# Optimization experiments

Measured on AMD Instinct MI355X. Metric: run time of the kernel, lower is better.

The kernel has to match this reference:

```python
import jax, jax.numpy as jnp
import numpy as np

L_LAYERS = 4
N_HEAD = 16
D_MODEL = 1024
D_K = 64
D_V = 64
D_HID = 4096
D_OUT = 10000
SEQ = 512
BATCH = 16
MASK_RATE = 0.15
LN_EPS = 1e-5


def sinusoid_table(n_position, model_size):
    pos = np.arange(n_position)[:, None]
    hid = np.arange(model_size)[None, :]
    angle = pos / np.power(10000, 2 * (hid // 2) / model_size)
    tab = np.array(angle)
    tab[:, 0::2] = np.sin(tab[:, 0::2])
    tab[:, 1::2] = np.cos(tab[:, 1::2])
    return jnp.asarray(tab, dtype=jnp.float32)


def layer_norm(x, w, b):
    mu = jnp.mean(x, axis=-1, keepdims=True)
    var = jnp.mean(jnp.square(x - mu), axis=-1, keepdims=True)
    return (x - mu) * jax.lax.rsqrt(var + LN_EPS) * w + b


def setup_inputs() -> dict:
    key = jax.random.key(0)
    ks = jax.random.split(key, 32)
    s = 0.02
    inp = {
        "x": jax.random.normal(ks[0], (SEQ, BATCH, D_MODEL), dtype=jnp.float32),
        "rnd": jax.random.uniform(ks[1], (BATCH, SEQ), dtype=jnp.float32),
        "posi": sinusoid_table(SEQ, D_MODEL),
        "ln0_w": jnp.ones((D_MODEL,), jnp.float32),
        "ln0_b": jnp.zeros((D_MODEL,), jnp.float32),
        # stacked per-layer params [L, ...]
        "Wq": jax.random.normal(ks[2], (L_LAYERS, N_HEAD * D_K, D_MODEL), jnp.float32) * np.sqrt(2.0 / (D_MODEL + D_K)),
        "bq": jnp.zeros((L_LAYERS, N_HEAD * D_K), jnp.float32),
        "Wk": jax.random.normal(ks[3], (L_LAYERS, N_HEAD * D_K, D_MODEL), jnp.float32) * np.sqrt(2.0 / (D_MODEL + D_K)),
        "bk": jnp.zeros((L_LAYERS, N_HEAD * D_K), jnp.float32),
        "Wv": jax.random.normal(ks[4], (L_LAYERS, N_HEAD * D_V, D_MODEL), jnp.float32) * np.sqrt(2.0 / (D_MODEL + D_V)),
        "bv": jnp.zeros((L_LAYERS, N_HEAD * D_V), jnp.float32),
        "Wfc": jax.random.normal(ks[5], (L_LAYERS, D_MODEL, N_HEAD * D_V), jnp.float32) * s,
        "bfc": jnp.zeros((L_LAYERS, D_MODEL), jnp.float32),
        "ln1_w": jnp.ones((L_LAYERS, D_MODEL), jnp.float32),
        "ln1_b": jnp.zeros((L_LAYERS, D_MODEL), jnp.float32),
        "W1": jax.random.normal(ks[6], (L_LAYERS, D_HID, D_MODEL), jnp.float32) * s,
        "b1": jnp.zeros((L_LAYERS, D_HID), jnp.float32),
        "W2": jax.random.normal(ks[7], (L_LAYERS, D_MODEL, D_HID), jnp.float32) * s,
        "b2": jnp.zeros((L_LAYERS, D_MODEL), jnp.float32),
        "ln2_w": jnp.ones((L_LAYERS, D_MODEL), jnp.float32),
        "ln2_b": jnp.zeros((L_LAYERS, D_MODEL), jnp.float32),
        "Wo": jax.random.normal(ks[8], (D_OUT, D_MODEL), jnp.float32) * s,
        "bo": jnp.zeros((D_OUT,), jnp.float32),
    }
    return inp


def reference(x, rnd, posi, ln0_w, ln0_b, Wq, bq, Wk, bk, Wv, bv, Wfc, bfc,
              ln1_w, ln1_b, W1, b1, W2, b2, ln2_w, ln2_b, Wo, bo):
    scale = 1.0 / np.sqrt(D_K)
    # [length, batch, d] -> [batch, length, d]
    h = jnp.transpose(x, (1, 0, 2))
    # random input masking: keep where rnd > mask_rate
    keep = (rnd > MASK_RATE).astype(h.dtype)  # [B, S]
    h = h * keep[:, :, None]
    enc = layer_norm(h, ln0_w, ln0_b) + posi[None, :, :]

    for l in range(L_LAYERS):
        residual = enc
        q = (enc @ Wq[l].T + bq[l]).reshape(BATCH, SEQ, N_HEAD, D_K)
        k = (enc @ Wk[l].T + bk[l]).reshape(BATCH, SEQ, N_HEAD, D_K)
        v = (enc @ Wv[l].T + bv[l]).reshape(BATCH, SEQ, N_HEAD, D_V)
        attn = jnp.einsum('bqhd,bkhd->bhqk', q, k) * scale
        attn = jax.nn.softmax(attn, axis=-1)
        out = jnp.einsum('bhqk,bkhd->bqhd', attn, v).reshape(BATCH, SEQ, N_HEAD * D_V)
        out = out @ Wfc[l].T + bfc[l]
        enc = layer_norm(out + residual, ln1_w[l], ln1_b[l])
        # position-wise FFN (conv1d kernel=1 == per-token linear)
        ff = jax.nn.relu(enc @ W1[l].T + b1[l]) @ W2[l].T + b2[l]
        enc = layer_norm(ff + enc, ln2_w[l], ln2_b[l])

    logits = enc @ Wo.T + bo  # [B, S, D_OUT]
    out = jax.nn.log_softmax(logits, axis=-1)
    return jnp.transpose(out, (1, 0, 2))  # [S, B, D_OUT]
```

## Files before the change

### kernel.cpp

```cpp
#include <hip/hip_runtime.h>
#include <cstdint>

typedef unsigned short u16;
typedef unsigned int u32;
typedef __attribute__((ext_vector_type(8))) short vs8;
typedef __attribute__((ext_vector_type(4))) short vs4;
typedef __attribute__((ext_vector_type(4))) float vf4;
typedef __attribute__((ext_vector_type(4))) float f32x4;

#define NLAYER 4
#define SEQ 512
#define BATCH 16
#define DM 1024
#define NTOK 8192
#define DOUT 10000
#define DOUTP 10240

static __device__ __forceinline__ u16 f2bf(float f) {
    u32 u = __float_as_uint(f);
    return (u16)((u + 0x7FFFu + ((u >> 16) & 1u)) >> 16);
}
static __device__ __forceinline__ float bf2f(u16 h) { return __uint_as_float((u32)h << 16); }

static __device__ __forceinline__ void gload16(const void* g, void* l) {
    __builtin_amdgcn_global_load_lds(
        (const __attribute__((address_space(1))) u32*)(uintptr_t)g,
        (__attribute__((address_space(3))) u32*)(u32)(uintptr_t)l, 16, 0, 0);
}

template <int BM, bool RELU, bool OUTBF>
__global__ __launch_bounds__(512, 1) void gemm2p(const u16* __restrict__ A, const u16* __restrict__ Bw,
                                                 const float* __restrict__ bias, void* __restrict__ Cv,
                                                 int N, int K, int nMt, int nNt)
{
    constexpr int LA = BM / 128;
    constexpr int LB = 2;
    constexpr int WCNT = 2 * (LA + LB);
    constexpr int MR = BM / 32;

    __shared__ __align__(16) u16 lds[2 * 2 * BM * 32 + 2 * 2 * 256 * 32];
    u16* As = lds;
    u16* Bs = lds + 2 * 2 * BM * 32;

    const int t = threadIdx.x;
    const int wid = t >> 6, lane = t & 63;
    const int lr = lane & 15, lg = lane >> 4;
    const int wr = wid >> 2, wc = wid & 3;
    const int wrb = wr * (BM / 2), wcb = wc * 64;
    const int slot8 = (lg ^ ((lr >> 1) & 3)) * 8;

    const int nwg = nMt * nNt;
    const int orig = blockIdx.x;
    const int q8 = nwg >> 3, r8 = nwg & 7;
    const int xcd = orig & 7, idx = orig >> 3;
    const int wg = ((xcd < r8) ? xcd * (q8 + 1) : r8 * (q8 + 1) + (xcd - r8) * q8) + idx;
    const int GN = 8;
    const int gsz = GN * nMt;
    const int grp = wg / gsz;
    const int rem = wg - grp * gsz;
    const int gw = min(GN, nNt - grp * GN);
    const int mt = rem / gw;
    const int nt = grp * GN + (rem - mt * gw);
    const size_t m0 = (size_t)mt * BM;
    const size_t n0 = (size_t)nt * 256;

    const int srow = wid * 16 + (lane >> 2);
    const int scg = (lane & 3) ^ ((lane >> 3) & 3);
    const u16* gA = A + (m0 + srow) * (size_t)K + scg * 8;
    const u16* gB = Bw + (n0 + srow) * (size_t)K + scg * 8;

    auto stageA = [&](int b, int kh, int kt) {
#pragma unroll
        for (int i = 0; i < LA; ++i)
            gload16(gA + (size_t)i * 128 * K + kt + kh * 32,
                    &As[(((b << 1) + kh) * BM + (i * 8 + wid) * 16) * 32]);
    };
    auto stageB = [&](int b, int kh, int kt) {
#pragma unroll
        for (int i = 0; i < LB; ++i)
            gload16(gB + (size_t)i * 128 * K + kt + kh * 32,
                    &Bs[(((b << 1) + kh) * 256 + (i * 8 + wid) * 16) * 32]);
    };
    auto ldA = [&](int i, int kk, int b) -> vs8 {
        return *(const vs8*)&As[(((b << 1) + kk) * BM + wrb + i * 16 + lr) * 32 + slot8];
    };
    auto ldB = [&](int j, int kk, int b) -> vs8 {
        return *(const vs8*)&Bs[(((b << 1) + kk) * 256 + wcb + j * 16 + lr) * 32 + slot8];
    };

    f32x4 acc[MR][4];
#pragma unroll
    for (int i = 0; i < MR; ++i)
#pragma unroll
        for (int j = 0; j < 4; ++j) acc[i][j] = (f32x4){0.f, 0.f, 0.f, 0.f};

    const int NT = K >> 6;

    stageA(0, 0, 0); stageB(0, 0, 0);
    stageA(0, 1, 0); stageB(0, 1, 0);
    stageA(1, 0, 64); stageB(1, 0, 64);
    if constexpr (WCNT == 8) asm volatile("s_waitcnt vmcnt(8)" ::: "memory");
    else                     asm volatile("s_waitcnt vmcnt(6)" ::: "memory");
    __builtin_amdgcn_s_barrier();

    for (int tt = 0; tt < NT; ++tt) {
        const int buf = tt & 1;
        const int ktn = min(tt + 1, NT - 1) << 6;
        const int ktn2 = min(tt + 2, NT - 1) << 6;
        vs8 af[MR], bf[4];

#pragma unroll
        for (int j = 0; j < 4; ++j) bf[j] = ldB(j, 0, buf);
#pragma unroll
        for (int i = 0; i < MR; ++i) af[i] = ldA(i, 0, buf);
        stageA(buf ^ 1, 1, ktn);
        stageB(buf ^ 1, 1, ktn);
        __builtin_amdgcn_s_barrier();
        asm volatile("s_waitcnt lgkmcnt(0)" ::: "memory");
        __builtin_amdgcn_sched_barrier(0);
        __builtin_amdgcn_s_setprio(1);
#pragma unroll
        for (int i = 0; i < MR; ++i)
#pragma unroll
            for (int j = 0; j < 4; ++j)
                acc[i][j] = __builtin_amdgcn_mfma_f32_16x16x32_bf16(bf[j], af[i], acc[i][j], 0, 0, 0);
        __builtin_amdgcn_s_setprio(0);
        if constexpr (WCNT == 8) asm volatile("s_waitcnt vmcnt(8)" ::: "memory");
        else                     asm volatile("s_waitcnt vmcnt(6)" ::: "memory");
        __builtin_amdgcn_s_barrier();

#pragma unroll
        for (int j = 0; j < 4; ++j) bf[j] = ldB(j, 1, buf);
#pragma unroll
        for (int i = 0; i < MR; ++i) af[i] = ldA(i, 1, buf);
        stageA(buf, 0, ktn2);
        stageB(buf, 0, ktn2);
        __builtin_amdgcn_s_barrier();
        asm volatile("s_waitcnt lgkmcnt(0)" ::: "memory");
        __builtin_amdgcn_sched_barrier(0);
        __builtin_amdgcn_s_setprio(1);
#pragma unroll
        for (int i = 0; i < MR; ++i)
#pragma unroll
            for (int j = 0; j < 4; ++j)
                acc[i][j] = __builtin_amdgcn_mfma_f32_16x16x32_bf16(bf[j], af[i], acc[i][j], 0, 0, 0);
        __builtin_amdgcn_s_setprio(0);
        if constexpr (WCNT == 8) asm volatile("s_waitcnt vmcnt(8)" ::: "memory");
        else                     asm volatile("s_waitcnt vmcnt(6)" ::: "memory");
        __builtin_amdgcn_s_barrier();
    }

    asm volatile("s_waitcnt vmcnt(0)" ::: "memory");

#pragma unroll
    for (int i = 0; i < MR; ++i) {
        const size_t cm = m0 + wrb + 16 * i + lr;
#pragma unroll
        for (int j = 0; j < 4; ++j) {
            const size_t cn = n0 + wcb + 16 * j + lg * 4;
            const vf4 bv4 = *(const vf4*)&bias[cn];
            f32x4 v = acc[i][j];
#pragma unroll
            for (int r = 0; r < 4; ++r) {
                v[r] += bv4[r];
                if (RELU) v[r] = fmaxf(v[r], 0.f);
            }
            if (OUTBF) {
                vs4 o;
#pragma unroll
                for (int r = 0; r < 4; ++r) o[r] = (short)f2bf(v[r]);
                *(vs4*)&((u16*)Cv)[cm * (size_t)N + cn] = o;
            } else {
                *(vf4*)&((float*)Cv)[cm * (size_t)N + cn] = v;
            }
        }
    }
}

__global__ __launch_bounds__(256) void vtrans_k(const u16* __restrict__ vb, u16* __restrict__ vt, int ldv)
{
    __shared__ u16 tile[64][80];
    const int t = threadIdx.x;
    const int bh = blockIdx.x >> 3, st = blockIdx.x & 7;
    const int b = bh >> 4, h = bh & 15;
    const int s0 = st * 64;
    {
        const int s = t >> 2, d0 = (t & 3) * 16;
        const vs8* src = (const vs8*)(vb + ((size_t)(b * 512 + s0 + s)) * ldv + h * 64 + d0);
        *(vs8*)&tile[s][d0] = src[0];
        *(vs8*)&tile[s][d0 + 8] = src[1];
    }
    __syncthreads();
    {
        const int d = t >> 2, r0 = (t & 3) * 16;
        u16 tmp[16];
#pragma unroll
        for (int i = 0; i < 16; ++i) tmp[i] = tile[r0 + i][d];
        vs8* dst = (vs8*)(vt + ((size_t)bh * 64 + d) * 512 + s0 + r0);
        dst[0] = *(const vs8*)&tmp[0];
        dst[1] = *(const vs8*)&tmp[8];
    }
}

__global__ __launch_bounds__(256) void attn_k(const u16* __restrict__ qb, const u16* __restrict__ kb,
                                              const u16* __restrict__ vtb, u16* __restrict__ ob, int ldq)
{
    __shared__ __align__(16) float SlF[32 * 520];
    const int t = threadIdx.x;
    const int wid = t >> 6, lane = t & 63;
    const int lr = lane & 15, lg = lane >> 4;
    const int bh = blockIdx.x >> 4, qt = blockIdx.x & 15;
    const int b = bh >> 4, h = bh & 15;
    const int q0 = qt * 32;

    vs8 aq[2][2];
#pragma unroll
    for (int i2 = 0; i2 < 2; ++i2)
#pragma unroll
        for (int kk = 0; kk < 2; ++kk)
            aq[i2][kk] = *(const vs8*)(qb + ((size_t)(b * 512 + q0 + 16 * i2 + lr)) * ldq + h * 64 + kk * 32 + lg * 8);

    f32x4 sa[2][8];
#pragma unroll
    for (int i2 = 0; i2 < 2; ++i2)
#pragma unroll
        for (int j = 0; j < 8; ++j) sa[i2][j] = (f32x4){0.f, 0.f, 0.f, 0.f};

#pragma unroll
    for (int j = 0; j < 8; ++j) {
        const int col = 128 * wid + 16 * j + lr;
#pragma unroll
        for (int kk = 0; kk < 2; ++kk) {
            vs8 bk = *(const vs8*)(kb + ((size_t)(b * 512 + col)) * ldq + h * 64 + kk * 32 + lg * 8);
#pragma unroll
            for (int i2 = 0; i2 < 2; ++i2)
                sa[i2][j] = __builtin_amdgcn_mfma_f32_16x16x32_bf16(bk, aq[i2][kk], sa[i2][j], 0, 0, 0);
        }
    }
#pragma unroll
    for (int i2 = 0; i2 < 2; ++i2)
#pragma unroll
        for (int j = 0; j < 8; ++j) {
            vf4 w;
#pragma unroll
            for (int r = 0; r < 4; ++r) w[r] = sa[i2][j][r] * 0.125f;
            *(vf4*)&SlF[(16 * i2 + lr) * 520 + 128 * wid + 16 * j + 4 * lg] = w;
        }
    __syncthreads();

    {
        const int row = t >> 3, seg = t & 7;
        const float* Sr = &SlF[row * 520 + seg * 64];
        float v[64];
        float m = -3.0e38f;
#pragma unroll
        for (int c = 0; c < 16; ++c) {
            const int cc = (c + row + seg) & 15;
            const vf4 w = *(const vf4*)&Sr[cc * 4];
#pragma unroll
            for (int e = 0; e < 4; ++e) { v[c * 4 + e] = w[e]; m = fmaxf(m, w[e]); }
        }
        m = fmaxf(m, __shfl_xor(m, 1));
        m = fmaxf(m, __shfl_xor(m, 2));
        m = fmaxf(m, __shfl_xor(m, 4));
        float s = 0.f;
#pragma unroll
        for (int i = 0; i < 64; ++i) { v[i] = __expf(v[i] - m); s += v[i]; }
        s += __shfl_xor(s, 1);
        s += __shfl_xor(s, 2);
        s += __shfl_xor(s, 4);
        const float inv = 1.f / s;
        u16* P16 = (u16*)SlF;
#pragma unroll
        for (int c = 0; c < 16; ++c) {
            const int cc = (c + row + seg) & 15;
            vs4 o;
#pragma unroll
            for (int e = 0; e < 4; ++e) o[e] = (short)f2bf(v[c * 4 + e] * inv);
            *(vs4*)&P16[row * 1040 + seg * 64 + cc * 4] = o;
        }
    }
    __syncthreads();

    const int rt = wid >> 1, ct0 = (wid & 1) * 2;
    f32x4 oa[2];
    oa[0] = (f32x4){0.f, 0.f, 0.f, 0.f};
    oa[1] = (f32x4){0.f, 0.f, 0.f, 0.f};
    const u16* P16 = (const u16*)SlF;
#pragma unroll
    for (int kt = 0; kt < 16; ++kt) {
        vs8 pa = *(const vs8*)&P16[(16 * rt + lr) * 1040 + kt * 32 + lg * 8];
#pragma unroll
        for (int c = 0; c < 2; ++c) {
            const int col = (ct0 + c) * 16 + lr;
            vs8 bv = *(const vs8*)(vtb + ((size_t)bh * 64 + col) * 512 + kt * 32 + lg * 8);
            oa[c] = __builtin_amdgcn_mfma_f32_16x16x32_bf16(bv, pa, oa[c], 0, 0, 0);
        }
    }
#pragma unroll
    for (int c = 0; c < 2; ++c) {
        const int qq = q0 + 16 * rt + lr;
        const int d0c = h * 64 + (ct0 + c) * 16 + lg * 4;
        vs4 o;
#pragma unroll
        for (int r = 0; r < 4; ++r) o[r] = (short)f2bf(oa[c][r]);
        *(vs4*)&ob[((size_t)b * 512 + qq) * 1024 + d0c] = o;
    }
}

__global__ __launch_bounds__(256) void embed_k(const float* __restrict__ x, const float* __restrict__ rnd,
                                               const float* __restrict__ posi, const float* __restrict__ w,
                                               const float* __restrict__ bb, u16* __restrict__ outb)
{
    const int tok = blockIdx.x;
    const int b = tok >> 9, s = tok & 511;
    const int t = threadIdx.x;
    const float keep = rnd[tok] > 0.15f ? 1.f : 0.f;
    vf4 xv = ((const vf4*)(x + ((size_t)s * 16 + b) * 1024))[t];
    xv *= keep;
    float s1 = xv[0] + xv[1] + xv[2] + xv[3];
    float s2 = xv[0] * xv[0] + xv[1] * xv[1] + xv[2] * xv[2] + xv[3] * xv[3];
#pragma unroll
    for (int mk = 1; mk < 64; mk <<= 1) { s1 += __shfl_xor(s1, mk); s2 += __shfl_xor(s2, mk); }
    __shared__ float red[8];
    if ((t & 63) == 0) { red[t >> 6] = s1; red[4 + (t >> 6)] = s2; }
    __syncthreads();
    s1 = red[0] + red[1] + red[2] + red[3];
    s2 = red[4] + red[5] + red[6] + red[7];
    const float mu = s1 * (1.f / 1024.f);
    const float var = s2 * (1.f / 1024.f) - mu * mu;
    const float rs = rsqrtf(var + 1e-5f);
    vf4 wv = ((const vf4*)w)[t];
    vf4 bv = ((const vf4*)bb)[t];
    vf4 pv = ((const vf4*)(posi + (size_t)s * 1024))[t];
    vs4 yb;
#pragma unroll
    for (int c = 0; c < 4; ++c)
        yb[c] = (short)f2bf((xv[c] - mu) * rs * wv[c] + bv[c] + pv[c]);
    *(vs4*)(outb + (size_t)tok * 1024 + t * 4) = yb;
}

__global__ __launch_bounds__(256) void add_ln_k(const u16* x, const u16* resid,
                                                const float* __restrict__ w, const float* __restrict__ bb,
                                                u16* out)
{
    const size_t row = blockIdx.x;
    const int t = threadIdx.x;
    const vs4 xv4 = *(const vs4*)(x + row * 1024 + t * 4);
    const vs4 rv4 = *(const vs4*)(resid + row * 1024 + t * 4);
    float xv[4];
#pragma unroll
    for (int c = 0; c < 4; ++c) xv[c] = bf2f((u16)xv4[c]) + bf2f((u16)rv4[c]);
    float s1 = xv[0] + xv[1] + xv[2] + xv[3];
    float s2 = xv[0] * xv[0] + xv[1] * xv[1] + xv[2] * xv[2] + xv[3] * xv[3];
#pragma unroll
    for (int mk = 1; mk < 64; mk <<= 1) { s1 += __shfl_xor(s1, mk); s2 += __shfl_xor(s2, mk); }
    __shared__ float red[8];
    if ((t & 63) == 0) { red[t >> 6] = s1; red[4 + (t >> 6)] = s2; }
    __syncthreads();
    s1 = red[0] + red[1] + red[2] + red[3];
    s2 = red[4] + red[5] + red[6] + red[7];
    const float mu = s1 * (1.f / 1024.f);
    const float var = s2 * (1.f / 1024.f) - mu * mu;
    const float rs = rsqrtf(var + 1e-5f);
    const vf4 wv = ((const vf4*)w)[t];
    const vf4 bv = ((const vf4*)bb)[t];
    vs4 yb;
#pragma unroll
    for (int c = 0; c < 4; ++c)
        yb[c] = (short)f2bf((xv[c] - mu) * rs * wv[c] + bv[c]);
    *(vs4*)(out + row * 1024 + t * 4) = yb;
}

__global__ __launch_bounds__(256) void logsm_k(const u16* __restrict__ lgts, float* __restrict__ out)
{
    const int tok = blockIdx.x;
    const int b = tok >> 9, s = tok & 511;
    const int t = threadIdx.x;
    const u16* row = lgts + (size_t)tok * DOUTP;
    float v[40];
    float m = -3.0e38f;
#pragma unroll
    for (int i = 0; i < 40; ++i) {
        const int c = t + 256 * i;
        v[i] = (c < DOUT) ? bf2f(row[c]) : -3.0e38f;
        m = fmaxf(m, v[i]);
    }
#pragma unroll
    for (int mk = 1; mk < 64; mk <<= 1) m = fmaxf(m, __shfl_xor(m, mk));
    __shared__ float red[8];
    if ((t & 63) == 0) red[t >> 6] = m;
    __syncthreads();
    m = fmaxf(fmaxf(red[0], red[1]), fmaxf(red[2], red[3]));
    float sum = 0.f;
#pragma unroll
    for (int i = 0; i < 40; ++i) sum += __expf(v[i] - m);
#pragma unroll
    for (int mk = 1; mk < 64; mk <<= 1) sum += __shfl_xor(sum, mk);
    if ((t & 63) == 0) red[4 + (t >> 6)] = sum;
    __syncthreads();
    sum = red[4] + red[5] + red[6] + red[7];
    const float ls = m + __logf(sum);
    float* orow = out + ((size_t)s * 16 + b) * DOUT;
#pragma unroll
    for (int i = 0; i < 40; ++i) {
        const int c = t + 256 * i;
        if (c < DOUT) __builtin_nontemporal_store(v[i] - ls, &orow[c]);
    }
}

__global__ void conv_k(const float* __restrict__ src, u16* __restrict__ dst, int n4)
{
    const int i = blockIdx.x * 256 + threadIdx.x;
    if (i >= n4) return;
    vf4 v = ((const vf4*)src)[i];
    vs4 o;
#pragma unroll
    for (int c = 0; c < 4; ++c) o[c] = (short)f2bf(v[c]);
    ((vs4*)dst)[i] = o;
}

__global__ void convq_k(const float* __restrict__ src, u16* __restrict__ dst, int n4, int perl4,
                        int dstl4, int off4)
{
    const int i = blockIdx.x * 256 + threadIdx.x;
    if (i >= n4) return;
    const int l = i / perl4, r = i - l * perl4;
    vf4 v = ((const vf4*)src)[i];
    vs4 o;
#pragma unroll
    for (int c = 0; c < 4; ++c) o[c] = (short)f2bf(v[c]);
    ((vs4*)dst)[(size_t)l * dstl4 + off4 + r] = o;
}

__global__ void biasq_k(const float* __restrict__ bq, const float* __restrict__ bk,
                        const float* __restrict__ bv, float* __restrict__ dst)
{
    const int i = blockIdx.x * 256 + threadIdx.x;
    const int l2 = i / 3072, c = i - l2 * 3072;
    float v;
    if (c < 1024) v = bq[l2 * 1024 + c];
    else if (c < 2048) v = bk[l2 * 1024 + c - 1024];
    else v = bv[l2 * 1024 + c - 2048];
    dst[i] = v;
}

__global__ void padwo_k(const float* __restrict__ src, u16* __restrict__ dst)
{
    const int i = blockIdx.x * 256 + threadIdx.x;
    const size_t e = (size_t)i * 4;
    const int r = (int)(e >> 10);
    vs4 o;
    if (r < DOUT) {
        vf4 v = *(const vf4*)(src + (size_t)r * 1024 + (e & 1023));
#pragma unroll
        for (int c = 0; c < 4; ++c) o[c] = (short)f2bf(v[c]);
    } else {
        o[0] = o[1] = o[2] = o[3] = 0;
    }
    *(vs4*)(dst + e) = o;
}

__global__ void padbo_k(const float* __restrict__ src, float* __restrict__ dst)
{
    const int i = blockIdx.x * 256 + threadIdx.x;
    if (i < DOUTP) dst[i] = (i < DOUT) ? src[i] : 0.f;
}

extern "C" void kernel_launch(void* const* d_in, const int* in_sizes, int n_in,
                              void* d_out, int out_size, void* d_ws, size_t ws_size,
                              hipStream_t stream)
{
    (void)in_sizes; (void)n_in; (void)out_size; (void)ws_size;
    const float* x     = (const float*)d_in[0];
    const float* rnd   = (const float*)d_in[1];
    const float* posi  = (const float*)d_in[2];
    const float* ln0_w = (const float*)d_in[3];
    const float* ln0_b = (const float*)d_in[4];
    const float* Wq    = (const float*)d_in[5];
    const float* bq    = (const float*)d_in[6];
    const float* Wk    = (const float*)d_in[7];
    const float* bk    = (const float*)d_in[8];
    const float* Wv    = (const float*)d_in[9];
    const float* bv    = (const float*)d_in[10];
    const float* Wfc   = (const float*)d_in[11];
    const float* bfc   = (const float*)d_in[12];
    const float* ln1_w = (const float*)d_in[13];
    const float* ln1_b = (const float*)d_in[14];
    const float* W1    = (const float*)d_in[15];
    const float* b1    = (const float*)d_in[16];
    const float* W2    = (const float*)d_in[17];
    const float* b2    = (const float*)d_in[18];
    const float* ln2_w = (const float*)d_in[19];
    const float* ln2_b = (const float*)d_in[20];
    const float* Wo    = (const float*)d_in[21];
    const float* bo    = (const float*)d_in[22];

    const size_t l1e = 1024 * 1024;
    const size_t l2e = 4096 * 1024;
    const size_t l3e = 3072 * 1024;

    char* p = (char*)d_ws;
    size_t off = 0;
    auto take = [&](size_t bytes) {
        char* r = p + off;
        off += (bytes + 255) & ~(size_t)255;
        return r;
    };
    u16*   Wqkv_b = (u16*)take(NLAYER * l3e * 2);
    u16*   Wfc_b  = (u16*)take(NLAYER * l1e * 2);
    u16*   W1_b   = (u16*)take(NLAYER * l2e * 2);
    u16*   W2_b   = (u16*)take(NLAYER * l2e * 2);
    u16*   Wo_b   = (u16*)take((size_t)DOUTP * DM * 2);
    float* bqkv_p = (float*)take(NLAYER * 3072 * 4);
    float* bo_p   = (float*)take(DOUTP * 4);
    u16*   enc_b  = (u16*)take((size_t)NTOK * DM * 2);
    char*  pool   = take((size_t)NTOK * DOUTP * 2);
    u16*   qkv_b  = (u16*)(pool);
    u16*   vt_b   = (u16*)(pool + 50331648);
    u16*   attn_b = (u16*)(pool + 67108864);
    u16*   fc_b   = (u16*)(pool);
    u16*   ff_b   = (u16*)(pool);
    u16*   ff2_b  = (u16*)(pool + 67108864);
    u16*   lgt_b  = (u16*)(pool);

    const dim3 blk(256);
    int n4;
    n4 = (int)(NLAYER * l1e / 4);
    convq_k<<<(n4 + 255) / 256, blk, 0, stream>>>(Wq, Wqkv_b, n4, 262144, 786432, 0);
    convq_k<<<(n4 + 255) / 256, blk, 0, stream>>>(Wk, Wqkv_b, n4, 262144, 786432, 262144);
    convq_k<<<(n4 + 255) / 256, blk, 0, stream>>>(Wv, Wqkv_b, n4, 262144, 786432, 524288);
    conv_k<<<(n4 + 255) / 256, blk, 0, stream>>>(Wfc, Wfc_b, n4);
    n4 = (int)(NLAYER * l2e / 4);
    conv_k<<<(n4 + 255) / 256, blk, 0, stream>>>(W1, W1_b, n4);
    conv_k<<<(n4 + 255) / 256, blk, 0, stream>>>(W2, W2_b, n4);
    padwo_k<<<(DOUTP * DM / 4) / 256, blk, 0, stream>>>(Wo, Wo_b);
    padbo_k<<<40, blk, 0, stream>>>(bo, bo_p);
    biasq_k<<<48, blk, 0, stream>>>(bq, bk, bv, bqkv_p);

    embed_k<<<NTOK, blk, 0, stream>>>(x, rnd, posi, ln0_w, ln0_b, enc_b);

    for (int l = 0; l < NLAYER; ++l) {
        gemm2p<128, false, true><<<768, 512, 0, stream>>>(enc_b, Wqkv_b + l * l3e, bqkv_p + l * 3072,
                                                          qkv_b, 3072, 1024, 64, 12);
        vtrans_k<<<2048, blk, 0, stream>>>(qkv_b + 2048, vt_b, 3072);
        attn_k<<<4096, blk, 0, stream>>>(qkv_b, qkv_b + 1024, vt_b, attn_b, 3072);
        gemm2p<128, false, true><<<256, 512, 0, stream>>>(attn_b, Wfc_b + l * l1e, bfc + l * 1024,
                                                          fc_b, 1024, 1024, 64, 4);
        add_ln_k<<<NTOK, blk, 0, stream>>>(fc_b, enc_b, ln1_w + l * 1024, ln1_b + l * 1024, enc_b);
        gemm2p<256, true, true><<<512, 512, 0, stream>>>(enc_b, W1_b + l * l2e, b1 + l * 4096,
                                                         ff_b, 4096, 1024, 32, 16);
        gemm2p<128, false, true><<<256, 512, 0, stream>>>(ff_b, W2_b + l * l2e, b2 + l * 1024,
                                                          ff2_b, 1024, 4096, 64, 4);
        add_ln_k<<<NTOK, blk, 0, stream>>>(ff2_b, enc_b, ln2_w + l * 1024, ln2_b + l * 1024, enc_b);
    }

    gemm2p<256, false, true><<<1280, 512, 0, stream>>>(enc_b, Wo_b, bo_p, lgt_b, DOUTP, 1024, 32, 40);
    logsm_k<<<NTOK, blk, 0, stream>>>(lgt_b, (float*)d_out);
}
```

Measured before the change: 2.086 ms.

## Fuse V transpose into GEMM epilogue, merge prep kernels, vectorize log-softmax

```diff
diff --git a/kernel.cpp b/kernel.cpp
--- a/kernel.cpp
+++ b/kernel.cpp
@@ -28,7 +28,7 @@
         (__attribute__((address_space(3))) u32*)(u32)(uintptr_t)l, 16, 0, 0);
 }
 
-template <int BM, bool RELU, bool OUTBF>
+template <int BM, bool RELU, bool OUTBF, bool TRV = false>
 __global__ __launch_bounds__(512, 1) void gemm2p(const u16* __restrict__ A, const u16* __restrict__ Bw,
                                                  const float* __restrict__ bias, void* __restrict__ Cv,
                                                  int N, int K, int nMt, int nNt)
@@ -122,8 +122,12 @@
 #pragma unroll
         for (int i = 0; i < MR; ++i)
 #pragma unroll
-            for (int j = 0; j < 4; ++j)
-                acc[i][j] = __builtin_amdgcn_mfma_f32_16x16x32_bf16(bf[j], af[i], acc[i][j], 0, 0, 0);
+            for (int j = 0; j < 4; ++j) {
+                if constexpr (TRV)
+                    acc[i][j] = __builtin_amdgcn_mfma_f32_16x16x32_bf16(af[i], bf[j], acc[i][j], 0, 0, 0);
+                else
+                    acc[i][j] = __builtin_amdgcn_mfma_f32_16x16x32_bf16(bf[j], af[i], acc[i][j], 0, 0, 0);
+            }
         __builtin_amdgcn_s_setprio(0);
         if constexpr (WCNT == 8) asm volatile("s_waitcnt vmcnt(8)" ::: "memory");
         else                     asm volatile("s_waitcnt vmcnt(6)" ::: "memory");
@@ -142,8 +146,12 @@
 #pragma unroll
         for (int i = 0; i < MR; ++i)
 #pragma unroll
-            for (int j = 0; j < 4; ++j)
-                acc[i][j] = __builtin_amdgcn_mfma_f32_16x16x32_bf16(bf[j], af[i], acc[i][j], 0, 0, 0);
+            for (int j = 0; j < 4; ++j) {
+                if constexpr (TRV)
+                    acc[i][j] = __builtin_amdgcn_mfma_f32_16x16x32_bf16(af[i], bf[j], acc[i][j], 0, 0, 0);
+                else
+                    acc[i][j] = __builtin_amdgcn_mfma_f32_16x16x32_bf16(bf[j], af[i], acc[i][j], 0, 0, 0);
+            }
         __builtin_amdgcn_s_setprio(0);
         if constexpr (WCNT == 8) asm volatile("s_waitcnt vmcnt(8)" ::: "memory");
         else                     asm volatile("s_waitcnt vmcnt(6)" ::: "memory");
@@ -152,53 +160,46 @@
 
     asm volatile("s_waitcnt vmcnt(0)" ::: "memory");
 
-#pragma unroll
-    for (int i = 0; i < MR; ++i) {
-        const size_t cm = m0 + wrb + 16 * i + lr;
-#pragma unroll
-        for (int j = 0; j < 4; ++j) {
-            const size_t cn = n0 + wcb + 16 * j + lg * 4;
-            const vf4 bv4 = *(const vf4*)&bias[cn];
-            f32x4 v = acc[i][j];
-#pragma unroll
-            for (int r = 0; r < 4; ++r) {
-                v[r] += bv4[r];
-                if (RELU) v[r] = fmaxf(v[r], 0.f);
+    if constexpr (TRV) {
+#pragma unroll
+        for (int i = 0; i < MR; ++i) {
+            const int cm0 = (int)m0 + wrb + 16 * i + lg * 4;
+            const int b_ = cm0 >> 9, s_ = cm0 & 511;
+#pragma unroll
+            for (int j = 0; j < 4; ++j) {
+                const int cn = (int)n0 + wcb + 16 * j + lr;
+                const float bval = bias[cn];
+                vs4 o;
+#pragma unroll
+                for (int r = 0; r < 4; ++r) o[r] = (short)f2bf(acc[i][j][r] + bval);
+                u16* dst = (u16*)Cv + (((size_t)(b_ * 16 + (cn >> 6))) * 64 + (cn & 63)) * 512 + s_;
+                *(vs4*)dst = o;
             }
-            if (OUTBF) {
-                vs4 o;
-#pragma unroll
-                for (int r = 0; r < 4; ++r) o[r] = (short)f2bf(v[r]);
-                *(vs4*)&((u16*)Cv)[cm * (size_t)N + cn] = o;
-            } else {
-                *(vf4*)&((float*)Cv)[cm * (size_t)N + cn] = v;
+        }
+    } else {
+#pragma unroll
+        for (int i = 0; i < MR; ++i) {
+            const size_t cm = m0 + wrb + 16 * i + lr;
+#pragma unroll
+            for (int j = 0; j < 4; ++j) {
+                const size_t cn = n0 + wcb + 16 * j + lg * 4;
+                const vf4 bv4 = *(const vf4*)&bias[cn];
+                f32x4 v = acc[i][j];
+#pragma unroll
+                for (int r = 0; r < 4; ++r) {
+                    v[r] += bv4[r];
+                    if (RELU) v[r] = fmaxf(v[r], 0.f);
+                }
+                if (OUTBF) {
+                    vs4 o;
+#pragma unroll
+                    for (int r = 0; r < 4; ++r) o[r] = (short)f2bf(v[r]);
+                    *(vs4*)&((u16*)Cv)[cm * (size_t)N + cn] = o;
+                } else {
+                    *(vf4*)&((float*)Cv)[cm * (size_t)N + cn] = v;
+                }
             }
         }
-    }
-}
-
-__global__ __launch_bounds__(256) void vtrans_k(const u16* __restrict__ vb, u16* __restrict__ vt, int ldv)
-{
-    __shared__ u16 tile[64][80];
-    const int t = threadIdx.x;
-    const int bh = blockIdx.x >> 3, st = blockIdx.x & 7;
-    const int b = bh >> 4, h = bh & 15;
-    const int s0 = st * 64;
-    {
-        const int s = t >> 2, d0 = (t & 3) * 16;
-        const vs8* src = (const vs8*)(vb + ((size_t)(b * 512 + s0 + s)) * ldv + h * 64 + d0);
-        *(vs8*)&tile[s][d0] = src[0];
-        *(vs8*)&tile[s][d0 + 8] = src[1];
-    }
-    __syncthreads();
-    {
-        const int d = t >> 2, r0 = (t & 3) * 16;
-        u16 tmp[16];
-#pragma unroll
-        for (int i = 0; i < 16; ++i) tmp[i] = tile[r0 + i][d];
-        vs8* dst = (vs8*)(vt + ((size_t)bh * 64 + d) * 512 + s0 + r0);
-        dst[0] = *(const vs8*)&tmp[0];
-        dst[1] = *(const vs8*)&tmp[8];
     }
 }
 
@@ -377,14 +378,19 @@
     const int tok = blockIdx.x;
     const int b = tok >> 9, s = tok & 511;
     const int t = threadIdx.x;
-    const u16* row = lgts + (size_t)tok * DOUTP;
+    const vs4* row4 = (const vs4*)(lgts + (size_t)tok * DOUTP);
     float v[40];
     float m = -3.0e38f;
 #pragma unroll
-    for (int i = 0; i < 40; ++i) {
-        const int c = t + 256 * i;
-        v[i] = (c < DOUT) ? bf2f(row[c]) : -3.0e38f;
-        m = fmaxf(m, v[i]);
+    for (int i = 0; i < 10; ++i) {
+        const int g = t + 256 * i;
+        const vs4 x4 = __builtin_nontemporal_load(row4 + g);
+#pragma unroll
+        for (int e = 0; e < 4; ++e) {
+            const float f = (g < 2500) ? bf2f((u16)x4[e]) : -3.0e38f;
+            v[i * 4 + e] = f;
+            m = fmaxf(m, f);
+        }
     }
 #pragma unroll
     for (int mk = 1; mk < 64; mk <<= 1) m = fmaxf(m, __shfl_xor(m, mk));
@@ -394,77 +400,87 @@
     m = fmaxf(fmaxf(red[0], red[1]), fmaxf(red[2], red[3]));
     float sum = 0.f;
 #pragma unroll
-    for (int i = 0; i < 40; ++i) sum += __expf(v[i] - m);
+    for (int i = 0; i < 40; ++i) { v[i] = __expf(v[i] - m); sum += v[i]; }
 #pragma unroll
     for (int mk = 1; mk < 64; mk <<= 1) sum += __shfl_xor(sum, mk);
     if ((t & 63) == 0) red[4 + (t >> 6)] = sum;
     __syncthreads();
     sum = red[4] + red[5] + red[6] + red[7];
     const float ls = m + __logf(sum);
-    float* orow = out + ((size_t)s * 16 + b) * DOUT;
-#pragma unroll
-    for (int i = 0; i < 40; ++i) {
-        const int c = t + 256 * i;
-        if (c < DOUT) __builtin_nontemporal_store(v[i] - ls, &orow[c]);
-    }
-}
-
-__global__ void conv_k(const float* __restrict__ src, u16* __restrict__ dst, int n4)
+    vf4* orow = (vf4*)(out + ((size_t)s * 16 + b) * DOUT);
+#pragma unroll
+    for (int i = 0; i < 10; ++i) {
+        const int g = t + 256 * i;
+        if (g < 2500) {
+            vf4 o;
+#pragma unroll
+            for (int e = 0; e < 4; ++e) o[e] = __logf(v[i * 4 + e]);
+            const float adj = m - ls;
+#pragma unroll
+            for (int e = 0; e < 4; ++e) o[e] = o[e] + adj;
+            __builtin_nontemporal_store(o, orow + g);
+        }
+    }
+}
+
+__global__ void prep_k(const float* __restrict__ Wq, const float* __restrict__ Wk,
+                       const float* __restrict__ Wv, const float* __restrict__ Wfc,
+                       const float* __restrict__ W1, const float* __restrict__ W2,
+                       const float* __restrict__ Wo, const float* __restrict__ bq,
+                       const float* __restrict__ bk, const float* __restrict__ bo,
+                       u16* __restrict__ Wqk_b, u16* __restrict__ Wv_b, u16* __restrict__ Wfc_b,
+                       u16* __restrict__ W1_b, u16* __restrict__ W2_b, u16* __restrict__ Wo_b,
+                       float* __restrict__ bqk_p, float* __restrict__ bo_p)
 {
     const int i = blockIdx.x * 256 + threadIdx.x;
-    if (i >= n4) return;
-    vf4 v = ((const vf4*)src)[i];
-    vs4 o;
-#pragma unroll
-    for (int c = 0; c < 4; ++c) o[c] = (short)f2bf(v[c]);
-    ((vs4*)dst)[i] = o;
-}
-
-__global__ void convq_k(const float* __restrict__ src, u16* __restrict__ dst, int n4, int perl4,
-                        int dstl4, int off4)
-{
-    const int i = blockIdx.x * 256 + threadIdx.x;
-    if (i >= n4) return;
-    const int l = i / perl4, r = i - l * perl4;
-    vf4 v = ((const vf4*)src)[i];
-    vs4 o;
-#pragma unroll
-    for (int c = 0; c < 4; ++c) o[c] = (short)f2bf(v[c]);
-    ((vs4*)dst)[(size_t)l * dstl4 + off4 + r] = o;
-}
-
-__global__ void biasq_k(const float* __restrict__ bq, const float* __restrict__ bk,
-                        const float* __restrict__ bv, float* __restrict__ dst)
-{
-    const int i = blockIdx.x * 256 + threadIdx.x;
-    const int l2 = i / 3072, c = i - l2 * 3072;
-    float v;
-    if (c < 1024) v = bq[l2 * 1024 + c];
-    else if (c < 2048) v = bk[l2 * 1024 + c - 1024];
-    else v = bv[l2 * 1024 + c - 2048];
-    dst[i] = v;
-}
-
-__global__ void padwo_k(const float* __restrict__ src, u16* __restrict__ dst)
-{
-    const int i = blockIdx.x * 256 + threadIdx.x;
-    const size_t e = (size_t)i * 4;
-    const int r = (int)(e >> 10);
-    vs4 o;
-    if (r < DOUT) {
-        vf4 v = *(const vf4*)(src + (size_t)r * 1024 + (e & 1023));
+    auto cvt = [](vf4 v) {
+        vs4 o;
 #pragma unroll
         for (int c = 0; c < 4; ++c) o[c] = (short)f2bf(v[c]);
+        return o;
+    };
+    if (i < 1048576) {
+        const int l = i >> 18, r = i & 262143;
+        ((vs4*)Wqk_b)[(size_t)l * 524288 + r] = cvt(((const vf4*)Wq)[i]);
+    } else if (i < 2097152) {
+        const int ii = i - 1048576;
+        const int l = ii >> 18, r = ii & 262143;
+        ((vs4*)Wqk_b)[(size_t)l * 524288 + 262144 + r] = cvt(((const vf4*)Wk)[ii]);
+    } else if (i < 3145728) {
+        const int ii = i - 2097152;
+        ((vs4*)Wv_b)[ii] = cvt(((const vf4*)Wv)[ii]);
+    } else if (i < 4194304) {
+        const int ii = i - 3145728;
+        ((vs4*)Wfc_b)[ii] = cvt(((const vf4*)Wfc)[ii]);
+    } else if (i < 8388608) {
+        const int ii = i - 4194304;
+        ((vs4*)W1_b)[ii] = cvt(((const vf4*)W1)[ii]);
+    } else if (i < 12582912) {
+        const int ii = i - 8388608;
+        ((vs4*)W2_b)[ii] = cvt(((const vf4*)W2)[ii]);
+    } else if (i < 15204352) {
+        const int ii = i - 12582912;
+        const size_t e = (size_t)ii * 4;
+        const int r = (int)(e >> 10);
+        vs4 o;
+        if (r < DOUT) o = cvt(*(const vf4*)(Wo + (size_t)r * 1024 + (e & 1023)));
+        else { o[0] = o[1] = o[2] = o[3] = 0; }
+        *(vs4*)(Wo_b + e) = o;
     } else {
-        o[0] = o[1] = o[2] = o[3] = 0;
-    }
-    *(vs4*)(dst + e) = o;
-}
-
-__global__ void padbo_k(const float* __restrict__ src, float* __restrict__ dst)
-{
-    const int i = blockIdx.x * 256 + threadIdx.x;
-    if (i < DOUTP) dst[i] = (i < DOUT) ? src[i] : 0.f;
+        const int ii = i - 15204352;
+        if (ii < 2048) {
+            const int f = ii * 4, l = f >> 11, c = f & 2047;
+            vf4 v = (c < 1024) ? *(const vf4*)&bq[l * 1024 + c]
+                               : *(const vf4*)&bk[l * 1024 + c - 1024];
+            *(vf4*)&bqk_p[f] = v;
+        } else {
+            const int f = (ii - 2048) * 4;
+            vf4 o;
+#pragma unroll
+            for (int e = 0; e < 4; ++e) o[e] = (f + e < DOUT) ? bo[f + e] : 0.f;
+            *(vf4*)&bo_p[f] = o;
+        }
+    }
 }
 
 extern "C" void kernel_launch(void* const* d_in, const int* in_sizes, int n_in,
@@ -496,10 +512,6 @@
     const float* Wo    = (const float*)d_in[21];
     const float* bo    = (const float*)d_in[22];
 
-    const size_t l1e = 1024 * 1024;
-    const size_t l2e = 4096 * 1024;
-    const size_t l3e = 3072 * 1024;
-
     char* p = (char*)d_ws;
     size_t off = 0;
     auto take = [&](size_t bytes) {
@@ -507,46 +519,39 @@
         off += (bytes + 255) & ~(size_t)255;
         return r;
     };
-    u16*   Wqkv_b = (u16*)take(NLAYER * l3e * 2);
-    u16*   Wfc_b  = (u16*)take(NLAYER * l1e * 2);
-    u16*   W1_b   = (u16*)take(NLAYER * l2e * 2);
-    u16*   W2_b   = (u16*)take(NLAYER * l2e * 2);
+    u16*   Wqk_b  = (u16*)take((size_t)NLAYER * 2048 * 1024 * 2);
+    u16*   Wv_b   = (u16*)take((size_t)NLAYER * 1024 * 1024 * 2);
+    u16*   Wfc_b  = (u16*)take((size_t)NLAYER * 1024 * 1024 * 2);
+    u16*   W1_b   = (u16*)take((size_t)NLAYER * 4096 * 1024 * 2);
+    u16*   W2_b   = (u16*)take((size_t)NLAYER * 4096 * 1024 * 2);
     u16*   Wo_b   = (u16*)take((size_t)DOUTP * DM * 2);
-    float* bqkv_p = (float*)take(NLAYER * 3072 * 4);
+    float* bqk_p  = (float*)take(NLAYER * 2048 * 4);
     float* bo_p   = (float*)take(DOUTP * 4);
     u16*   enc_b  = (u16*)take((size_t)NTOK * DM * 2);
     char*  pool   = take((size_t)NTOK * DOUTP * 2);
     u16*   qkv_b  = (u16*)(pool);
-    u16*   vt_b   = (u16*)(pool + 50331648);
-    u16*   attn_b = (u16*)(pool + 67108864);
+    u16*   vt_b   = (u16*)(pool + 33554432);
+    u16*   attn_b = (u16*)(pool + 50331648);
     u16*   fc_b   = (u16*)(pool);
     u16*   ff_b   = (u16*)(pool);
     u16*   ff2_b  = (u16*)(pool + 67108864);
     u16*   lgt_b  = (u16*)(pool);
 
     const dim3 blk(256);
-    int n4;
-    n4 = (int)(NLAYER * l1e / 4);
-    convq_k<<<(n4 + 255) / 256, blk, 0, stream>>>(Wq, Wqkv_b, n4, 262144, 786432, 0);
-    convq_k<<<(n4 + 255) / 256, blk, 0, stream>>>(Wk, Wqkv_b, n4, 262144, 786432, 262144);
-    convq_k<<<(n4 + 255) / 256, blk, 0, stream>>>(Wv, Wqkv_b, n4, 262144, 786432, 524288);
-    conv_k<<<(n4 + 255) / 256, blk, 0, stream>>>(Wfc, Wfc_b, n4);
-    n4 = (int)(NLAYER * l2e / 4);
-    conv_k<<<(n4 + 255) / 256, blk, 0, stream>>>(W1, W1_b, n4);
-    conv_k<<<(n4 + 255) / 256, blk, 0, stream>>>(W2, W2_b, n4);
-    padwo_k<<<(DOUTP * DM / 4) / 256, blk, 0, stream>>>(Wo, Wo_b);
-    padbo_k<<<40, blk, 0, stream>>>(bo, bo_p);
-    biasq_k<<<48, blk, 0, stream>>>(bq, bk, bv, bqkv_p);
+    prep_k<<<59410, blk, 0, stream>>>(Wq, Wk, Wv, Wfc, W1, W2, Wo, bq, bk, bo,
+                                      Wqk_b, Wv_b, Wfc_b, W1_b, W2_b, Wo_b, bqk_p, bo_p);
 
     embed_k<<<NTOK, blk, 0, stream>>>(x, rnd, posi, ln0_w, ln0_b, enc_b);
 
+    const size_t l2e = 4096 * 1024;
     for (int l = 0; l < NLAYER; ++l) {
-        gemm2p<128, false, true><<<768, 512, 0, stream>>>(enc_b, Wqkv_b + l * l3e, bqkv_p + l * 3072,
-                                                          qkv_b, 3072, 1024, 64, 12);
-        vtrans_k<<<2048, blk, 0, stream>>>(qkv_b + 2048, vt_b, 3072);
-        attn_k<<<4096, blk, 0, stream>>>(qkv_b, qkv_b + 1024, vt_b, attn_b, 3072);
-        gemm2p<128, false, true><<<256, 512, 0, stream>>>(attn_b, Wfc_b + l * l1e, bfc + l * 1024,
-                                                          fc_b, 1024, 1024, 64, 4);
+        gemm2p<256, false, true><<<256, 512, 0, stream>>>(enc_b, Wqk_b + (size_t)l * 2097152,
+                                                          bqk_p + l * 2048, qkv_b, 2048, 1024, 32, 8);
+        gemm2p<128, false, true, true><<<256, 512, 0, stream>>>(enc_b, Wv_b + (size_t)l * 1048576,
+                                                                bv + l * 1024, vt_b, 1024, 1024, 64, 4);
+        attn_k<<<4096, blk, 0, stream>>>(qkv_b, qkv_b + 1024, vt_b, attn_b, 2048);
+        gemm2p<128, false, true><<<256, 512, 0, stream>>>(attn_b, Wfc_b + (size_t)l * 1048576,
+                                                          bfc + l * 1024, fc_b, 1024, 1024, 64, 4);
         add_ln_k<<<NTOK, blk, 0, stream>>>(fc_b, enc_b, ln1_w + l * 1024, ln1_b + l * 1024, enc_b);
         gemm2p<256, true, true><<<512, 512, 0, stream>>>(enc_b, W1_b + l * l2e, b1 + l * 4096,
                                                          ff_b, 4096, 1024, 32, 16);
```

Measured after the change: 1.955 ms. 1.07x faster.
